# Performance work log

Measured on AMD Instinct MI355X. Metric: run time of the kernel, lower is better.

## Reference

```python
import jax, jax.numpy as jnp
import numpy as np

D_MODEL = 512
NUM_HEADS = 8
D_K = D_MODEL // NUM_HEADS


def setup_inputs() -> dict:
    key = jax.random.key(0)
    ks = jax.random.split(key, 9)
    B, N = 4, 2048
    x = jax.random.normal(ks[0], (B, N, D_MODEL), dtype=jnp.float32)
    s = 1.0 / np.sqrt(D_MODEL)
    Wq = jax.random.normal(ks[1], (D_MODEL, D_MODEL), dtype=jnp.float32) * s
    bq = jax.random.normal(ks[2], (D_MODEL,), dtype=jnp.float32) * 0.02
    Wk = jax.random.normal(ks[3], (D_MODEL, D_MODEL), dtype=jnp.float32) * s
    bk = jax.random.normal(ks[4], (D_MODEL,), dtype=jnp.float32) * 0.02
    Wv = jax.random.normal(ks[5], (D_MODEL, D_MODEL), dtype=jnp.float32) * s
    bv = jax.random.normal(ks[6], (D_MODEL,), dtype=jnp.float32) * 0.02
    Wo = jax.random.normal(ks[7], (D_MODEL, D_MODEL), dtype=jnp.float32) * s
    bo = jax.random.normal(ks[8], (D_MODEL,), dtype=jnp.float32) * 0.02
    return {"x": x, "Wq": Wq, "bq": bq, "Wk": Wk, "bk": bk,
            "Wv": Wv, "bv": bv, "Wo": Wo, "bo": bo}


def reference(x, Wq, bq, Wk, bk, Wv, bv, Wo, bo):
    B, N, _ = x.shape
    # project and split heads: [B, H, N, d_k]
    def split_heads(t):
        return t.reshape(B, N, NUM_HEADS, D_K).transpose(0, 2, 1, 3)
    Q = split_heads(x @ Wq + bq)
    K = split_heads(x @ Wk + bk)
    V = split_heads(x @ Wv + bv)
    scale = 1.0 / np.sqrt(D_K)
    scores = jnp.einsum('bhqd,bhkd->bhqk', Q, K) * scale  # [B,H,N,N]
    probs = jax.nn.softmax(scores, axis=-1)
    attn = jnp.einsum('bhqk,bhkd->bhqd', probs, V)
    attn = attn.transpose(0, 2, 1, 3).reshape(B, N, D_MODEL)
    return attn @ Wo + bo
```

## Files before the change

### kernel.cpp

```cpp
#include <hip/hip_runtime.h>
#include <math.h>

#define D_MODEL 512
#define N_SEQ   2048
#define H       8
#define DK      64
#define NQT     (N_SEQ / 128)

typedef __attribute__((ext_vector_type(8)))  short bf16x8;
typedef __attribute__((ext_vector_type(4)))  float f32x4;
typedef __attribute__((ext_vector_type(16))) float f32x16;

__device__ __forceinline__ unsigned short f2b(float f) {
    unsigned int u = __float_as_uint(f);
    u += 0x7FFF + ((u >> 16) & 1);
    return (unsigned short)(u >> 16);
}

__device__ __forceinline__ unsigned int pack2(float lo, float hi) {
#if __has_builtin(__builtin_amdgcn_cvt_pk_bf16_f32)
    typedef __attribute__((ext_vector_type(2))) short bf16x2;
    bf16x2 p = __builtin_amdgcn_cvt_pk_bf16_f32(lo, hi);
    return (unsigned int)(unsigned short)p[0] |
           ((unsigned int)(unsigned short)p[1] << 16);
#else
    return (unsigned int)f2b(lo) | ((unsigned int)f2b(hi) << 16);
#endif
}

__device__ __forceinline__ float fexp2(float x) {
#if __has_builtin(__builtin_amdgcn_exp2f)
    return __builtin_amdgcn_exp2f(x);
#else
    return __expf(x * 0.6931471805599453f);
#endif
}

#define SC2 0.18033688011112042f

__global__ void transpose_all(
    const float* __restrict__ W0, const float* __restrict__ W1,
    const float* __restrict__ W2, const float* __restrict__ W3,
    unsigned short* __restrict__ T0, unsigned short* __restrict__ T1,
    unsigned short* __restrict__ T2, unsigned short* __restrict__ T3)
{
    const float* W; unsigned short* Wt;
    if      (blockIdx.z == 0) { W = W0; Wt = T0; }
    else if (blockIdx.z == 1) { W = W1; Wt = T1; }
    else if (blockIdx.z == 2) { W = W2; Wt = T2; }
    else                      { W = W3; Wt = T3; }

    __shared__ float t[32][33];
    const int tx = threadIdx.x, ty = threadIdx.y;
    const int x = blockIdx.x * 32 + tx;
    const int y0 = blockIdx.y * 32;
    for (int i = ty; i < 32; i += 8)
        t[i][tx] = W[(size_t)(y0 + i) * D_MODEL + x];
    __syncthreads();
    const int ox = blockIdx.y * 32 + tx;
    const int oy0 = blockIdx.x * 32;
    for (int i = ty; i < 32; i += 8)
        Wt[(size_t)(oy0 + i) * D_MODEL + ox] = f2b(t[tx][i]);
}

template<int AMODE, int SWAP>
__device__ __forceinline__ void gemm_body(
    const void* __restrict__ Aptr,
    const unsigned short* __restrict__ Wt,
    const float* __restrict__ bias,
    void* __restrict__ out, int mode, int bx, int by, float sc)
{
    __shared__ unsigned short As[128][72];
    __shared__ unsigned short Bs[128][72];

    const int tid  = threadIdx.x;
    const int lane = tid & 63, wave = tid >> 6;
    const int m0 = by * 128, n0 = bx * 128;
    const int wm = (wave & 1) * 64, wn = (wave >> 1) * 64;
    const int cn = lane & 15, g = lane >> 4;

    const int srow = tid >> 1;
    const int scol = (tid & 1) * 32;
    const float* Agf = (const float*)Aptr + (size_t)(m0 + srow) * D_MODEL + scol;
    const unsigned short* Agb =
        (const unsigned short*)Aptr + (size_t)(m0 + srow) * D_MODEL + scol;
    const unsigned short* Bg = Wt + (size_t)(n0 + srow) * D_MODEL + scol;

    f32x4 acc[4][4];
    #pragma unroll
    for (int i = 0; i < 4; ++i)
        #pragma unroll
        for (int j = 0; j < 4; ++j)
            acc[i][j] = (f32x4){0.f, 0.f, 0.f, 0.f};

    for (int k0 = 0; k0 < D_MODEL; k0 += 64) {
        bf16x8 av[4], bv[4];
        #pragma unroll
        for (int q = 0; q < 4; ++q) {
            if (AMODE) {
                float4 f0 = *(const float4*)(Agf + k0 + q * 8);
                float4 f1 = *(const float4*)(Agf + k0 + q * 8 + 4);
                unsigned int* pv = (unsigned int*)&av[q];
                pv[0] = pack2(f0.x, f0.y); pv[1] = pack2(f0.z, f0.w);
                pv[2] = pack2(f1.x, f1.y); pv[3] = pack2(f1.z, f1.w);
            } else {
                av[q] = *(const bf16x8*)(Agb + k0 + q * 8);
            }
            bv[q] = *(const bf16x8*)(Bg + k0 + q * 8);
        }
        __syncthreads();
        #pragma unroll
        for (int q = 0; q < 4; ++q) {
            *(bf16x8*)&As[srow][scol + q * 8] = av[q];
            *(bf16x8*)&Bs[srow][scol + q * 8] = bv[q];
        }
        __syncthreads();

        #pragma unroll
        for (int ks = 0; ks < 2; ++ks) {
            bf16x8 af[4], bf[4];
            #pragma unroll
            for (int i = 0; i < 4; ++i)
                af[i] = *(const bf16x8*)&As[wm + i * 16 + cn][ks * 32 + g * 8];
            #pragma unroll
            for (int j = 0; j < 4; ++j)
                bf[j] = *(const bf16x8*)&Bs[wn + j * 16 + cn][ks * 32 + g * 8];
            #pragma unroll
            for (int i = 0; i < 4; ++i)
                #pragma unroll
                for (int j = 0; j < 4; ++j) {
                    if (SWAP)
                        acc[i][j] = __builtin_amdgcn_mfma_f32_16x16x32_bf16(
                            bf[j], af[i], acc[i][j], 0, 0, 0);
                    else
                        acc[i][j] = __builtin_amdgcn_mfma_f32_16x16x32_bf16(
                            af[i], bf[j], acc[i][j], 0, 0, 0);
                }
        }
    }

    if constexpr (SWAP) {
        unsigned short* o = (unsigned short*)out;
        #pragma unroll
        for (int j = 0; j < 4; ++j) {
            const int dbase = n0 + wn + j * 16 + g * 4;
            const int hh = dbase >> 6, dd = dbase & 63;
            float4 bb = *(const float4*)&bias[dbase];
            #pragma unroll
            for (int i = 0; i < 4; ++i) {
                const int tt = m0 + wm + i * 16 + cn;
                const int bi = tt >> 11, tok = tt & (N_SEQ - 1);
                ushort4 pk;
                pk.x = f2b((acc[i][j][0] + bb.x) * sc);
                pk.y = f2b((acc[i][j][1] + bb.y) * sc);
                pk.z = f2b((acc[i][j][2] + bb.z) * sc);
                pk.w = f2b((acc[i][j][3] + bb.w) * sc);
                *(ushort4*)(o + (((size_t)bi * H + hh) * N_SEQ + tok) * DK + dd) = pk;
            }
        }
    } else if (mode == 2) {
        float* o = (float*)out;
        #pragma unroll
        for (int j = 0; j < 4; ++j) {
            const int n = n0 + wn + j * 16 + cn;
            const float bb = bias[n];
            #pragma unroll
            for (int i = 0; i < 4; ++i)
                #pragma unroll
                for (int r = 0; r < 4; ++r) {
                    const int m = m0 + wm + i * 16 + g * 4 + r;
                    o[(size_t)m * D_MODEL + n] = acc[i][j][r] + bb;
                }
        }
    } else {
        unsigned short* o = (unsigned short*)out;
        #pragma unroll
        for (int j = 0; j < 4; ++j) {
            const int n = n0 + wn + j * 16 + cn;
            const int h = n >> 6, d = n & 63;
            const float bb = bias[n];
            #pragma unroll
            for (int i = 0; i < 4; ++i) {
                const int m = m0 + wm + i * 16 + g * 4;
                const int b = m >> 11, t = m & (N_SEQ - 1);
                ushort4 pk;
                pk.x = f2b(acc[i][j][0] + bb);
                pk.y = f2b(acc[i][j][1] + bb);
                pk.z = f2b(acc[i][j][2] + bb);
                pk.w = f2b(acc[i][j][3] + bb);
                *(ushort4*)(o + (((size_t)b * H + h) * DK + d) * N_SEQ + t) = pk;
            }
        }
    }
}

__global__ __launch_bounds__(256) void gemm_qkv(
    const float* __restrict__ x,
    const unsigned short* __restrict__ Wtq,
    const unsigned short* __restrict__ Wtk,
    const unsigned short* __restrict__ Wtv,
    const float* __restrict__ bq, const float* __restrict__ bk,
    const float* __restrict__ bv,
    unsigned short* __restrict__ Qb, unsigned short* __restrict__ Kb,
    unsigned short* __restrict__ Vtb)
{
    if (blockIdx.z == 0)
        gemm_body<1, 1>(x, Wtq, bq, Qb, 0, blockIdx.x, blockIdx.y, SC2);
    else if (blockIdx.z == 1)
        gemm_body<1, 1>(x, Wtk, bk, Kb, 0, blockIdx.x, blockIdx.y, 1.0f);
    else
        gemm_body<1, 0>(x, Wtv, bv, Vtb, 1, blockIdx.x, blockIdx.y, 1.0f);
}

__global__ __launch_bounds__(256) void gemm_o(
    const unsigned short* __restrict__ A,
    const unsigned short* __restrict__ Wt,
    const float* __restrict__ bias, float* __restrict__ out)
{
    gemm_body<0, 0>(A, Wt, bias, out, 2, blockIdx.x, blockIdx.y, 1.0f);
}

__global__ __launch_bounds__(256, 4) void attn_mfma(
    const unsigned short* __restrict__ Q,
    const unsigned short* __restrict__ K,
    const unsigned short* __restrict__ Vt,
    float* __restrict__ Op, float* __restrict__ lp, int nb)
{
    __shared__ unsigned short Ks[64][72];
    __shared__ unsigned short Vs[64][72];

    const int tid = threadIdx.x, lane = tid & 63, wave = tid >> 6;
    const int qt = blockIdx.x, h = blockIdx.y;
    const int b = blockIdx.z >> 1, sp = blockIdx.z & 1;
    const int lq = lane & 31, hf = lane >> 5;
    const int q0 = qt * 128;

    const size_t hb = (size_t)b * H + h;
    const unsigned short* Qp = Q  + hb * N_SEQ * DK;
    const unsigned short* Kp = K  + hb * N_SEQ * DK;
    const unsigned short* Vp = Vt + hb * DK * N_SEQ;

    const int qs = q0 + wave * 32;
    bf16x8 qf[4];
    #pragma unroll
    for (int kd = 0; kd < 4; ++kd)
        qf[kd] = *(const bf16x8*)(Qp + (size_t)(qs + lq) * DK + kd * 16 + hf * 8);

    f32x16 O[2];
    #pragma unroll
    for (int r = 0; r < 16; ++r) { O[0][r] = 0.f; O[1][r] = 0.f; }
    float lacc = 0.f;

    const int krow = tid >> 2, kcol = (tid & 3) * 16;
    const int j0beg = sp * (N_SEQ / 2);

    for (int j0 = j0beg; j0 < j0beg + N_SEQ / 2; j0 += 64) {
        bf16x8 kv0 = *(const bf16x8*)(Kp + (size_t)(j0 + krow) * DK + kcol);
        bf16x8 kv1 = *(const bf16x8*)(Kp + (size_t)(j0 + krow) * DK + kcol + 8);
        bf16x8 vv0 = *(const bf16x8*)(Vp + (size_t)krow * N_SEQ + j0 + kcol);
        bf16x8 vv1 = *(const bf16x8*)(Vp + (size_t)krow * N_SEQ + j0 + kcol + 8);
        __syncthreads();
        *(bf16x8*)&Ks[krow][kcol]     = kv0;
        *(bf16x8*)&Ks[krow][kcol + 8] = kv1;
        *(bf16x8*)&Vs[krow][kcol]     = vv0;
        *(bf16x8*)&Vs[krow][kcol + 8] = vv1;
        __syncthreads();

        f32x16 s0, s1;
        #pragma unroll
        for (int r = 0; r < 16; ++r) { s0[r] = 0.f; s1[r] = 0.f; }
        #pragma unroll
        for (int kd = 0; kd < 4; ++kd) {
            bf16x8 a0 = *(const bf16x8*)&Ks[lq][kd * 16 + hf * 8];
            bf16x8 a1 = *(const bf16x8*)&Ks[32 + lq][kd * 16 + hf * 8];
            s0 = __builtin_amdgcn_mfma_f32_32x32x16_bf16(a0, qf[kd], s0, 0, 0, 0);
            s1 = __builtin_amdgcn_mfma_f32_32x32x16_bf16(a1, qf[kd], s1, 0, 0, 0);
        }

        unsigned int pk0[4][2], pk1[4][2];
        #pragma unroll
        for (int c = 0; c < 4; ++c)
            #pragma unroll
            for (int p = 0; p < 2; ++p) {
                pk0[c][p] = pack2(fexp2(s0[4 * c + 2 * p]),
                                  fexp2(s0[4 * c + 2 * p + 1]));
                pk1[c][p] = pack2(fexp2(s1[4 * c + 2 * p]),
                                  fexp2(s1[4 * c + 2 * p + 1]));
            }

        #pragma unroll
        for (int c = 0; c < 4; ++c)
            #pragma unroll
            for (int p = 0; p < 2; ++p) {
                lacc += __uint_as_float(pk0[c][p] << 16) +
                        __uint_as_float(pk0[c][p] & 0xFFFF0000u) +
                        __uint_as_float(pk1[c][p] << 16) +
                        __uint_as_float(pk1[c][p] & 0xFFFF0000u);
            }

        #pragma unroll
        for (int ks = 0; ks < 4; ++ks) {
            const unsigned int (*src)[2] = (ks < 2) ? pk0 : pk1;
            const int k2 = ks & 1;
            const unsigned int a0u = src[2 * k2 + hf][0];
            const unsigned int a1u = src[2 * k2 + hf][1];
            const unsigned int b0u = src[2 * k2 + 1 - hf][0];
            const unsigned int b1u = src[2 * k2 + 1 - hf][1];
            const unsigned int e0 = (unsigned int)__shfl_xor((int)b0u, 32);
            const unsigned int e1 = (unsigned int)__shfl_xor((int)b1u, 32);
            bf16x8 bp;
            unsigned int* bpu = (unsigned int*)&bp;
            bpu[0] = hf ? e0 : a0u;
            bpu[1] = hf ? e1 : a1u;
            bpu[2] = hf ? a0u : e0;
            bpu[3] = hf ? a1u : e1;
            bf16x8 va0 = *(const bf16x8*)&Vs[lq][ks * 16 + hf * 8];
            bf16x8 va1 = *(const bf16x8*)&Vs[32 + lq][ks * 16 + hf * 8];
            O[0] = __builtin_amdgcn_mfma_f32_32x32x16_bf16(va0, bp, O[0], 0, 0, 0);
            O[1] = __builtin_amdgcn_mfma_f32_32x32x16_bf16(va1, bp, O[1], 0, 0, 0);
        }
    }

    const size_t pbase =
        ((((size_t)sp * nb + b) * H + h) * NQT + qt) * (size_t)(64 * 128);
    #pragma unroll
    for (int dt = 0; dt < 2; ++dt)
        #pragma unroll
        for (int r = 0; r < 16; ++r) {
            const int row = (r & 3) + 8 * (r >> 2) + 4 * hf;
            Op[pbase + (size_t)(dt * 32 + row) * 128 + wave * 32 + lq] = O[dt][r];
        }
    const float lt = lacc + __shfl_xor(lacc, 32);
    if (hf == 0)
        lp[(((size_t)sp * nb + b) * H + h) * N_SEQ + q0 + wave * 32 + lq] = lt;
}

__global__ __launch_bounds__(256) void reduce_ctx(
    const float* __restrict__ Op, const float* __restrict__ lp,
    unsigned short* __restrict__ ctx, int nb)
{
    __shared__ float R[64][129];
    const int tid = threadIdx.x;
    const int qt = blockIdx.x, h = blockIdx.y, b = blockIdx.z;
    const size_t tile = (size_t)64 * 128;
    const size_t i0 = (((size_t)b * H + h) * NQT + qt) * tile;
    const size_t i1 = ((((size_t)nb + b) * H + h) * NQT + qt) * tile;

    #pragma unroll 4
    for (int u = 0; u < 32; ++u) {
        const int idx = u * 256 + tid;
        R[idx >> 7][idx & 127] = Op[i0 + idx] + Op[i1 + idx];
    }
    __syncthreads();

    const int q = tid & 127, dh = tid >> 7;
    const size_t lb = ((size_t)b * H + h) * N_SEQ + qt * 128 + q;
    const float inv = 1.0f / (lp[lb] + lp[(size_t)nb * H * N_SEQ + lb]);

    unsigned short* orow = ctx + ((size_t)b * N_SEQ + qt * 128 + q) * D_MODEL
                               + h * DK + dh * 32;
    #pragma unroll
    for (int t2 = 0; t2 < 4; ++t2) {
        unsigned int w[4];
        #pragma unroll
        for (int p = 0; p < 4; ++p)
            w[p] = pack2(R[dh * 32 + t2 * 8 + 2 * p][q] * inv,
                         R[dh * 32 + t2 * 8 + 2 * p + 1][q] * inv);
        *(bf16x8*)(orow + t2 * 8) = *(bf16x8*)w;
    }
}

extern "C" void kernel_launch(void* const* d_in, const int* in_sizes, int n_in,
                              void* d_out, int out_size, void* d_ws, size_t ws_size,
                              hipStream_t stream)
{
    const float* x  = (const float*)d_in[0];
    const float* Wq = (const float*)d_in[1];
    const float* bq = (const float*)d_in[2];
    const float* Wk = (const float*)d_in[3];
    const float* bk = (const float*)d_in[4];
    const float* Wv = (const float*)d_in[5];
    const float* bv = (const float*)d_in[6];
    const float* Wo = (const float*)d_in[7];
    const float* bo = (const float*)d_in[8];
    float* out = (float*)d_out;

    const int M = in_sizes[0] / D_MODEL;
    const int nb = M / N_SEQ;
    const size_t NX = (size_t)M * D_MODEL;
    const size_t NW = (size_t)D_MODEL * D_MODEL;

    unsigned short* Wtq = (unsigned short*)d_ws;
    unsigned short* Wtk = Wtq + NW;
    unsigned short* Wtv = Wtk + NW;
    unsigned short* Wto = Wtv + NW;
    unsigned short* Qb  = Wto + NW;
    unsigned short* Kb  = Qb + NX;
    unsigned short* Vtb = Kb + NX;
    float* Op = (float*)(Vtb + NX);
    float* lp = Op + (size_t)2 * nb * H * NQT * 8192;
    unsigned short* ctx = Qb;

    transpose_all<<<dim3(16, 16, 4), dim3(32, 8), 0, stream>>>(
        Wq, Wk, Wv, Wo, Wtq, Wtk, Wtv, Wto);

    gemm_qkv<<<dim3(D_MODEL / 128, M / 128, 3), 256, 0, stream>>>(
        x, Wtq, Wtk, Wtv, bq, bk, bv, Qb, Kb, Vtb);
    attn_mfma<<<dim3(NQT, H, nb * 2), 256, 0, stream>>>(Qb, Kb, Vtb, Op, lp, nb);
    reduce_ctx<<<dim3(NQT, H, nb), 256, 0, stream>>>(Op, lp, ctx, nb);
    gemm_o<<<dim3(D_MODEL / 128, M / 128), 256, 0, stream>>>(ctx, Wto, bo, out);
}
```

Baseline: 217.4 us.

## Fuse split-KV attention halves and reduction into one 512-thread block

The two KV-split halves now run as two groups of four waves inside one 512-thread block, and their partial outputs are combined through shared memory. This removes the separate reduce_ctx kernel and the global round-trip of fp32 partial outputs. The row sum of probabilities is now computed with an extra MFMA against a ones vector, and V is pre-swizzled when staged into LDS so the cross-half shuffle is no longer needed. The cost is one more MFMA per step and larger blocks with only half the grid, which could lower occupancy or parallelism.

New measurement: 190.4 us. -12.4%, faster.

```diff
diff --git a/kernel.cpp b/kernel.cpp
--- a/kernel.cpp
+++ b/kernel.cpp
@@ -220,50 +220,68 @@
     gemm_body<0, 0>(A, Wt, bias, out, 2, blockIdx.x, blockIdx.y, 1.0f);
 }
 
-__global__ __launch_bounds__(256, 4) void attn_mfma(
+__global__ __launch_bounds__(512, 4) void attn_mfma(
     const unsigned short* __restrict__ Q,
     const unsigned short* __restrict__ K,
     const unsigned short* __restrict__ Vt,
-    float* __restrict__ Op, float* __restrict__ lp, int nb)
-{
-    __shared__ unsigned short Ks[64][72];
-    __shared__ unsigned short Vs[64][72];
+    unsigned short* __restrict__ ctx)
+{
+    __shared__ unsigned short SM[2][2][64][72];
 
     const int tid = threadIdx.x, lane = tid & 63, wave = tid >> 6;
-    const int qt = blockIdx.x, h = blockIdx.y;
-    const int b = blockIdx.z >> 1, sp = blockIdx.z & 1;
+    const int qt = blockIdx.x, h = blockIdx.y, b = blockIdx.z;
+    const int sp = wave >> 2;
+    const int w4 = wave & 3;
     const int lq = lane & 31, hf = lane >> 5;
     const int q0 = qt * 128;
+    const int qs = q0 + w4 * 32;
 
     const size_t hb = (size_t)b * H + h;
     const unsigned short* Qp = Q  + hb * N_SEQ * DK;
     const unsigned short* Kp = K  + hb * N_SEQ * DK;
     const unsigned short* Vp = Vt + hb * DK * N_SEQ;
 
-    const int qs = q0 + wave * 32;
     bf16x8 qf[4];
     #pragma unroll
     for (int kd = 0; kd < 4; ++kd)
         qf[kd] = *(const bf16x8*)(Qp + (size_t)(qs + lq) * DK + kd * 16 + hf * 8);
 
-    f32x16 O[2];
+    f32x16 O[2], Ol;
     #pragma unroll
-    for (int r = 0; r < 16; ++r) { O[0][r] = 0.f; O[1][r] = 0.f; }
-    float lacc = 0.f;
-
-    const int krow = tid >> 2, kcol = (tid & 3) * 16;
-    const int j0beg = sp * (N_SEQ / 2);
-
-    for (int j0 = j0beg; j0 < j0beg + N_SEQ / 2; j0 += 64) {
+    for (int r = 0; r < 16; ++r) { O[0][r] = 0.f; O[1][r] = 0.f; Ol[r] = 0.f; }
+
+    bf16x8 onesA;
+    {
+        const short v = (lq == 0) ? (short)0x3F80 : (short)0;
+        #pragma unroll
+        for (int j = 0; j < 8; ++j) onesA[j] = v;
+    }
+
+    const int tl = tid & 255;
+    const int krow = tl >> 2, kcol = (tl & 3) * 16;
+    unsigned short (*Ks)[72] = SM[sp][0];
+    unsigned short (*Vs)[72] = SM[sp][1];
+
+    for (int it = 0; it < 16; ++it) {
+        const int j0 = sp * (N_SEQ / 2) + it * 64;
         bf16x8 kv0 = *(const bf16x8*)(Kp + (size_t)(j0 + krow) * DK + kcol);
         bf16x8 kv1 = *(const bf16x8*)(Kp + (size_t)(j0 + krow) * DK + kcol + 8);
         bf16x8 vv0 = *(const bf16x8*)(Vp + (size_t)krow * N_SEQ + j0 + kcol);
         bf16x8 vv1 = *(const bf16x8*)(Vp + (size_t)krow * N_SEQ + j0 + kcol + 8);
+        bf16x8 sw0, sw1;
+        {
+            ushort4* a = (ushort4*)&vv0;
+            ushort4* c = (ushort4*)&vv1;
+            ushort4* s0p = (ushort4*)&sw0;
+            ushort4* s1p = (ushort4*)&sw1;
+            s0p[0] = a[0]; s0p[1] = c[0];
+            s1p[0] = a[1]; s1p[1] = c[1];
+        }
         __syncthreads();
         *(bf16x8*)&Ks[krow][kcol]     = kv0;
         *(bf16x8*)&Ks[krow][kcol + 8] = kv1;
-        *(bf16x8*)&Vs[krow][kcol]     = vv0;
-        *(bf16x8*)&Vs[krow][kcol + 8] = vv1;
+        *(bf16x8*)&Vs[krow][kcol]     = sw0;
+        *(bf16x8*)&Vs[krow][kcol + 8] = sw1;
         __syncthreads();
 
         f32x16 s0, s1;
@@ -289,84 +307,59 @@
             }
 
         #pragma unroll
-        for (int c = 0; c < 4; ++c)
-            #pragma unroll
-            for (int p = 0; p < 2; ++p) {
-                lacc += __uint_as_float(pk0[c][p] << 16) +
-                        __uint_as_float(pk0[c][p] & 0xFFFF0000u) +
-                        __uint_as_float(pk1[c][p] << 16) +
-                        __uint_as_float(pk1[c][p] & 0xFFFF0000u);
-            }
-
-        #pragma unroll
         for (int ks = 0; ks < 4; ++ks) {
             const unsigned int (*src)[2] = (ks < 2) ? pk0 : pk1;
-            const int k2 = ks & 1;
-            const unsigned int a0u = src[2 * k2 + hf][0];
-            const unsigned int a1u = src[2 * k2 + hf][1];
-            const unsigned int b0u = src[2 * k2 + 1 - hf][0];
-            const unsigned int b1u = src[2 * k2 + 1 - hf][1];
-            const unsigned int e0 = (unsigned int)__shfl_xor((int)b0u, 32);
-            const unsigned int e1 = (unsigned int)__shfl_xor((int)b1u, 32);
+            const int c2 = (ks & 1) * 2;
             bf16x8 bp;
             unsigned int* bpu = (unsigned int*)&bp;
-            bpu[0] = hf ? e0 : a0u;
-            bpu[1] = hf ? e1 : a1u;
-            bpu[2] = hf ? a0u : e0;
-            bpu[3] = hf ? a1u : e1;
+            bpu[0] = src[c2][0];     bpu[1] = src[c2][1];
+            bpu[2] = src[c2 + 1][0]; bpu[3] = src[c2 + 1][1];
             bf16x8 va0 = *(const bf16x8*)&Vs[lq][ks * 16 + hf * 8];
             bf16x8 va1 = *(const bf16x8*)&Vs[32 + lq][ks * 16 + hf * 8];
             O[0] = __builtin_amdgcn_mfma_f32_32x32x16_bf16(va0, bp, O[0], 0, 0, 0);
             O[1] = __builtin_amdgcn_mfma_f32_32x32x16_bf16(va1, bp, O[1], 0, 0, 0);
-        }
-    }
-
-    const size_t pbase =
-        ((((size_t)sp * nb + b) * H + h) * NQT + qt) * (size_t)(64 * 128);
-    #pragma unroll
-    for (int dt = 0; dt < 2; ++dt)
-        #pragma unroll
-        for (int r = 0; r < 16; ++r) {
-            const int row = (r & 3) + 8 * (r >> 2) + 4 * hf;
-            Op[pbase + (size_t)(dt * 32 + row) * 128 + wave * 32 + lq] = O[dt][r];
-        }
-    const float lt = lacc + __shfl_xor(lacc, 32);
-    if (hf == 0)
-        lp[(((size_t)sp * nb + b) * H + h) * N_SEQ + q0 + wave * 32 + lq] = lt;
-}
-
-__global__ __launch_bounds__(256) void reduce_ctx(
-    const float* __restrict__ Op, const float* __restrict__ lp,
-    unsigned short* __restrict__ ctx, int nb)
-{
-    __shared__ float R[64][129];
-    const int tid = threadIdx.x;
-    const int qt = blockIdx.x, h = blockIdx.y, b = blockIdx.z;
-    const size_t tile = (size_t)64 * 128;
-    const size_t i0 = (((size_t)b * H + h) * NQT + qt) * tile;
-    const size_t i1 = ((((size_t)nb + b) * H + h) * NQT + qt) * tile;
-
-    #pragma unroll 4
-    for (int u = 0; u < 32; ++u) {
-        const int idx = u * 256 + tid;
-        R[idx >> 7][idx & 127] = Op[i0 + idx] + Op[i1 + idx];
-    }
+            Ol   = __builtin_amdgcn_mfma_f32_32x32x16_bf16(onesA, bp, Ol, 0, 0, 0);
+        }
+    }
+
+    float* R    = (float*)&SM[0][0][0][0];
+    float* Laux = R + 4 * 64 * 32;
+
     __syncthreads();
-
-    const int q = tid & 127, dh = tid >> 7;
-    const size_t lb = ((size_t)b * H + h) * N_SEQ + qt * 128 + q;
-    const float inv = 1.0f / (lp[lb] + lp[(size_t)nb * H * N_SEQ + lb]);
-
-    unsigned short* orow = ctx + ((size_t)b * N_SEQ + qt * 128 + q) * D_MODEL
-                               + h * DK + dh * 32;
-    #pragma unroll
-    for (int t2 = 0; t2 < 4; ++t2) {
-        unsigned int w[4];
-        #pragma unroll
-        for (int p = 0; p < 4; ++p)
-            w[p] = pack2(R[dh * 32 + t2 * 8 + 2 * p][q] * inv,
-                         R[dh * 32 + t2 * 8 + 2 * p + 1][q] * inv);
-        *(bf16x8*)(orow + t2 * 8) = *(bf16x8*)w;
+    if (sp == 1) {
+        #pragma unroll
+        for (int dt = 0; dt < 2; ++dt)
+            #pragma unroll
+            for (int r = 0; r < 16; ++r) {
+                const int d = (r & 3) + 8 * (r >> 2) + 4 * hf + 32 * dt;
+                R[(w4 * 64 + d) * 32 + lq] = O[dt][r];
+            }
+        if (hf == 0) Laux[w4 * 32 + lq] = Ol[0];
+    }
+    __syncthreads();
+    if (sp == 0) {
+        #pragma unroll
+        for (int dt = 0; dt < 2; ++dt)
+            #pragma unroll
+            for (int r = 0; r < 16; ++r) {
+                const int d = (r & 3) + 8 * (r >> 2) + 4 * hf + 32 * dt;
+                O[dt][r] += R[(w4 * 64 + d) * 32 + lq];
+            }
+        const float lsum = Ol[0] + Laux[w4 * 32 + lq];
+        const float linv = 1.0f / __shfl(lsum, lq);
+
+        unsigned short* ob = ctx + ((size_t)b * N_SEQ + qs + lq) * D_MODEL
+                                 + h * DK + hf * 4;
+        #pragma unroll
+        for (int dt = 0; dt < 2; ++dt)
+            #pragma unroll
+            for (int c = 0; c < 4; ++c) {
+                unsigned int w2[2];
+                w2[0] = pack2(O[dt][4 * c + 0] * linv, O[dt][4 * c + 1] * linv);
+                w2[1] = pack2(O[dt][4 * c + 2] * linv, O[dt][4 * c + 3] * linv);
+                *(unsigned int*)(ob + dt * 32 + c * 8)     = w2[0];
+                *(unsigned int*)(ob + dt * 32 + c * 8 + 2) = w2[1];
+            }
     }
 }
 
@@ -397,16 +390,13 @@
     unsigned short* Qb  = Wto + NW;
     unsigned short* Kb  = Qb + NX;
     unsigned short* Vtb = Kb + NX;
-    float* Op = (float*)(Vtb + NX);
-    float* lp = Op + (size_t)2 * nb * H * NQT * 8192;
-    unsigned short* ctx = Qb;
+    unsigned short* ctx = Vtb + NX;
 
     transpose_all<<<dim3(16, 16, 4), dim3(32, 8), 0, stream>>>(
         Wq, Wk, Wv, Wo, Wtq, Wtk, Wtv, Wto);
 
     gemm_qkv<<<dim3(D_MODEL / 128, M / 128, 3), 256, 0, stream>>>(
         x, Wtq, Wtk, Wtv, bq, bk, bv, Qb, Kb, Vtb);
-    attn_mfma<<<dim3(NQT, H, nb * 2), 256, 0, stream>>>(Qb, Kb, Vtb, Op, lp, nb);
-    reduce_ctx<<<dim3(NQT, H, nb), 256, 0, stream>>>(Op, lp, ctx, nb);
+    attn_mfma<<<dim3(NQT, H, nb), 512, 0, stream>>>(Qb, Kb, Vtb, ctx);
     gemm_o<<<dim3(D_MODEL / 128, M / 128), 256, 0, stream>>>(ctx, Wto, bo, out);
 }
```
